# Optimization experiments

Measured on AMD Instinct MI355X. Metric: run time of the kernel, lower is better.

## Reference

```python
import jax, jax.numpy as jnp
import numpy as np

N = 262144
C = 81
NUM_HARD = 32768


def setup_inputs() -> dict:
    key = jax.random.key(0)
    k1, k2, k3, k4 = jax.random.split(key, 4)
    return {
        "cls_score": jax.random.normal(k1, (N, C), dtype=jnp.float32),
        "rois_label": jax.random.randint(k2, (N,), 0, C, dtype=jnp.int32),
        "bbox_pred": jax.random.normal(k3, (N, 4), dtype=jnp.float32),
        "rois_target": jax.random.normal(k4, (N, 4), dtype=jnp.float32),
        "rois_inside_ws": jnp.ones((N, 4), dtype=jnp.float32),
        "rois_outside_ws": jnp.ones((N, 4), dtype=jnp.float32),
        "num_hard": NUM_HARD,
    }


def reference(cls_score, rois_label, bbox_pred, rois_target,
              rois_inside_ws, rois_outside_ws, num_hard):
    num_classes = cls_score.shape[1]
    pos = rois_label > 0                                   # [N] bool
    num_pos = jnp.sum(pos.astype(jnp.float32))

    # --- hard-example mining on detached scores (no grad through selection) ---
    conf_p = jax.lax.stop_gradient(cls_score)              # [N, C]
    x_max = jnp.max(conf_p)                                # global scalar max (as in torch code)
    lse = jnp.log(jnp.sum(jnp.exp(conf_p - x_max), axis=1)) + x_max   # [N]
    gathered = jnp.take_along_axis(conf_p, rois_label[:, None].astype(jnp.int32), axis=1)[:, 0]
    loss_c = lse - gathered                                # [N]
    loss_c = jnp.where(pos, jnp.float32(100.0), loss_c)    # force positives in
    _, topk_idx = jax.lax.top_k(loss_c, num_hard)          # [num_hard]

    # --- weighted cross entropy on selected hard examples ---
    weight = jnp.ones((num_classes,), dtype=jnp.float32).at[0].set(num_pos / num_hard)
    sel_logits = cls_score[topk_idx]                       # [num_hard, C]
    sel_labels = rois_label[topk_idx]                      # [num_hard]
    logp = jax.nn.log_softmax(sel_logits, axis=1)
    nll = -jnp.take_along_axis(logp, sel_labels[:, None].astype(jnp.int32), axis=1)[:, 0]
    w = weight[sel_labels]
    loss_cls = jnp.sum(w * nll) / jnp.sum(w)               # torch weighted-mean CE

    # --- smooth L1 on positive rois only (masked; mean over num_pos*4 elems) ---
    diff = bbox_pred - rois_target                         # [N, 4]
    ad = jnp.abs(diff)
    sl1 = jnp.where(ad < 1.0, 0.5 * diff * diff, ad - 0.5)
    posf = pos.astype(sl1.dtype)[:, None]
    loss_box = jnp.sum(sl1 * posf) / (num_pos * 4.0)

    return loss_cls, loss_box
```

## Files before the change

kernel.cpp:

```cpp
#include <hip/hip_runtime.h>

#define NROWS 262144
#define NCLS  81
#define NTILES 4096
#define TILE_FLOATS 5184
#define KEY100 0xC2C80000u

struct ScalarBlk {
    unsigned mode;
    unsigned num_pos;
};

__device__ __forceinline__ unsigned mono(float f) {
    unsigned u = __float_as_uint(f);
    return (u & 0x80000000u) ? ~u : (u | 0x80000000u);
}

__global__ __launch_bounds__(256) void row_kernel(
        const float* __restrict__ cls, const int* __restrict__ label,
        const float* __restrict__ bpred, const float* __restrict__ btgt,
        float* __restrict__ nll_out,
        unsigned* __restrict__ npPart, unsigned* __restrict__ ngPart,
        unsigned* __restrict__ nePart, float* __restrict__ gtPart,
        float* __restrict__ pnPart, float* __restrict__ boxPart)
{
    __shared__ float sm[TILE_FLOATS];
    __shared__ int slbl[64];
    __shared__ unsigned wnp[4], wng[4], wne[4];
    __shared__ float wgt_[4], wpn[4], wbs[4];

    const int t   = threadIdx.x;
    const int blk = blockIdx.x;

    const float4* src = (const float4*)(cls + (size_t)blk * TILE_FLOATS);
    float4* dst = (float4*)sm;
    #pragma unroll
    for (int jj = 0; jj < 5; ++jj) dst[t + 256*jj] = src[t + 256*jj];
    if (t < 16) dst[t + 1280] = src[t + 1280];
    if (t < 64) slbl[t] = label[blk*64 + t];
    __syncthreads();

    const int row = t >> 2;
    const int j   = t & 3;
    const float* rp = sm + row * NCLS;

    float s = 0.f;
    for (int i = j; i < NCLS; i += 4) s += __expf(rp[i]);
    s += __shfl_xor(s, 1);
    s += __shfl_xor(s, 2);

    unsigned pcnt = 0, gcnt = 0, ecnt = 0;
    float gtv = 0.f, pnv = 0.f;
    if (j == 0) {
        float lse = __logf(s);
        int r = blk*64 + row;
        int lbl = slbl[row];
        bool pos = lbl > 0;
        float nll = lse - rp[lbl];
        float loss_c = pos ? 100.0f : nll;
        unsigned k = mono(loss_c);
        nll_out[r] = nll;
        pcnt = pos ? 1u : 0u;
        gcnt = (k > KEY100) ? 1u : 0u;
        ecnt = (!pos && k == KEY100) ? 1u : 0u;
        gtv  = (k > KEY100) ? nll : 0.f;
        pnv  = pos ? nll : 0.f;
    }

    float bsum = 0.f;
    {
        int gi = blk*256 + t;
        float p = bpred[gi], q = btgt[gi];
        if (slbl[row] > 0) {
            float d = p - q, ad = fabsf(d);
            bsum = (ad < 1.f) ? 0.5f*d*d : ad - 0.5f;
        }
    }

    #pragma unroll
    for (int off = 32; off; off >>= 1) {
        pcnt += __shfl_xor(pcnt, off);
        gcnt += __shfl_xor(gcnt, off);
        ecnt += __shfl_xor(ecnt, off);
        gtv  += __shfl_xor(gtv, off);
        pnv  += __shfl_xor(pnv, off);
        bsum += __shfl_xor(bsum, off);
    }
    const int lane = t & 63, wid = t >> 6;
    if (lane == 0) {
        wnp[wid] = pcnt; wng[wid] = gcnt; wne[wid] = ecnt;
        wgt_[wid] = gtv; wpn[wid] = pnv; wbs[wid] = bsum;
    }
    __syncthreads();
    if (t == 0) {
        npPart[blk]  = wnp[0]+wnp[1]+wnp[2]+wnp[3];
        ngPart[blk]  = wng[0]+wng[1]+wng[2]+wng[3];
        nePart[blk]  = wne[0]+wne[1]+wne[2]+wne[3];
        gtPart[blk]  = wgt_[0]+wgt_[1]+wgt_[2]+wgt_[3];
        pnPart[blk]  = wpn[0]+wpn[1]+wpn[2]+wpn[3];
        boxPart[blk] = wbs[0]+wbs[1]+wbs[2]+wbs[3];
    }
}

__global__ __launch_bounds__(1024) void fast_finalize(
        const unsigned* __restrict__ npPart, const unsigned* __restrict__ ngPart,
        const unsigned* __restrict__ nePart, const float* __restrict__ gtPart,
        const float* __restrict__ pnPart, const float* __restrict__ boxPart,
        const int* __restrict__ label, const float* __restrict__ nll,
        const int* __restrict__ d_num_hard, ScalarBlk* __restrict__ sc,
        float* __restrict__ out)
{
    const int t = threadIdx.x, lane = t & 63, wid = t >> 6;
    __shared__ unsigned wNp[16], wNg[16], wNe[16];
    __shared__ float wPn[16], wGt[16], wBx[16];
    __shared__ unsigned sCross, sCumBefore;
    __shared__ float sFull, sPartial;

    uint4  np = ((const uint4*)npPart)[t];
    uint4  ng = ((const uint4*)ngPart)[t];
    uint4  ne = ((const uint4*)nePart)[t];
    float4 gt = ((const float4*)gtPart)[t];
    float4 pn = ((const float4*)pnPart)[t];
    float4 bx = ((const float4*)boxPart)[t];
    unsigned myNp = np.x+np.y+np.z+np.w;
    unsigned myNg = ng.x+ng.y+ng.z+ng.w;
    unsigned myNe = ne.x+ne.y+ne.z+ne.w;
    float myGt = gt.x+gt.y+gt.z+gt.w;
    float myPn = pn.x+pn.y+pn.z+pn.w;
    float myBx = bx.x+bx.y+bx.z+bx.w;

    unsigned incNp = myNp; float incPn = myPn;
    #pragma unroll
    for (int off = 1; off < 64; off <<= 1) {
        unsigned v = __shfl_up(incNp, off);
        float    f = __shfl_up(incPn, off);
        if (lane >= off) { incNp += v; incPn += f; }
    }
    #pragma unroll
    for (int off = 32; off; off >>= 1) {
        myNg += __shfl_xor(myNg, off);
        myNe += __shfl_xor(myNe, off);
        myGt += __shfl_xor(myGt, off);
        myBx += __shfl_xor(myBx, off);
    }
    if (lane == 63) { wNp[wid] = incNp; wPn[wid] = incPn; }
    if (lane == 0)  { wNg[wid] = myNg; wNe[wid] = myNe; wGt[wid] = myGt; wBx[wid] = myBx; }
    __syncthreads();

    unsigned NP = 0, NG = 0, NE = 0; float GT = 0.f, BX = 0.f;
    unsigned npOff = 0; float pnOff = 0.f;
    for (int w = 0; w < 16; ++w) {
        NP += wNp[w]; NG += wNg[w]; NE += wNe[w]; GT += wGt[w]; BX += wBx[w];
        if (w < wid) { npOff += wNp[w]; pnOff += wPn[w]; }
    }
    const unsigned k = (unsigned)(*d_num_hard);
    const bool fast = (NG < k) && (NG + NP >= k) && (NE == 0);
    if (t == 0) { sc->mode = fast ? 1u : 0u; sc->num_pos = NP; }

    if (fast) {
        const unsigned need = k - NG;
        unsigned E = npOff + incNp - myNp;
        float    F = pnOff + incPn - myPn;
        unsigned a[4] = { np.x, np.y, np.z, np.w };
        float    p4[4] = { pn.x, pn.y, pn.z, pn.w };
        unsigned cum = E; float fl = F;
        #pragma unroll
        for (int i = 0; i < 4; ++i) {
            if (cum < need && cum + a[i] >= need) {
                sCross = (unsigned)(4*t + i); sCumBefore = cum; sFull = fl;
            }
            cum += a[i]; fl += p4[i];
        }
    }
    __syncthreads();
    if (!fast) return;

    const unsigned need = k - NG;
    if (t < 64) {
        int r = (int)sCross * 64 + t;
        int lbl = label[r];
        float v = nll[r];
        bool pos = lbl > 0;
        unsigned long long b = __ballot(pos);
        unsigned rank = (unsigned)__popcll(b & ((1ull << t) - 1ull));
        unsigned rem = need - sCumBefore;
        float c = (pos && rank < rem) ? v : 0.f;
        #pragma unroll
        for (int off = 32; off; off >>= 1) c += __shfl_xor(c, off);
        if (t == 0) sPartial = c;
    }
    __syncthreads();
    if (t == 0) {
        float wgt0 = (float)NP / (float)k;
        float num = wgt0 * GT + sFull + sPartial;
        float den = wgt0 * (float)NG + (float)need;
        out[0] = num / den;
        out[1] = BX / ((float)NP * 4.0f);
    }
}

__device__ void scan_desc_64k(const unsigned* hist, unsigned k,
                              unsigned* outB, unsigned* outRem,
                              unsigned* wsum )
{
    const int t = threadIdx.x, lane = t & 63, wid = t >> 6;
    unsigned sum = 0;
    for (int j = 0; j < 64; ++j) sum += hist[65535 - (t*64 + j)];
    unsigned inc = sum;
    #pragma unroll
    for (int off = 1; off < 64; off <<= 1) {
        unsigned v = __shfl_up(inc, off);
        if (lane >= off) inc += v;
    }
    if (lane == 63) wsum[wid] = inc;
    __syncthreads();
    unsigned woff = 0;
    for (int w = 0; w < wid; ++w) woff += wsum[w];
    unsigned running = woff + inc - sum;
    for (int j = 0; j < 64; ++j) {
        unsigned bkt = 65535u - (unsigned)(t*64 + j);
        unsigned c = hist[bkt];
        if (running < k && running + c >= k) { *outB = bkt; *outRem = k - running; }
        running += c;
    }
}

__global__ __launch_bounds__(1024) void slow_fallback(
        const int* __restrict__ label, const float* __restrict__ nll,
        const float* __restrict__ boxPart, const int* __restrict__ d_num_hard,
        const ScalarBlk* __restrict__ sc, unsigned* __restrict__ hist,
        float* __restrict__ out)
{
    if (sc->mode) return;
    const int t = threadIdx.x, lane = t & 63, wid = t >> 6;
    const unsigned k = (unsigned)(*d_num_hard);
    const unsigned NP = sc->num_pos;
    __shared__ unsigned wsum[16];
    __shared__ unsigned sB1, sKrem, sTkey, sNeed;
    __shared__ unsigned wEq[16];
    __shared__ float r1[16], r2[16], r3[16];

    for (int i = t; i < 65536; i += 1024) hist[i] = 0u;
    __syncthreads();
    for (int base = 0; base < NROWS; base += 1024) {
        int r = base + t;
        int lbl = label[r]; float v = nll[r];
        unsigned key = mono(lbl > 0 ? 100.0f : v);
        unsigned bkt = key >> 16;
        unsigned long long active = __ballot(1);
        while (active) {
            int leader = (int)__builtin_ctzll(active);
            unsigned lb = __shfl(bkt, leader);
            unsigned long long grp = __ballot(bkt == lb) & active;
            if (lane == leader) atomicAdd(&hist[lb], (unsigned)__popcll(grp));
            active &= ~grp;
        }
    }
    __syncthreads();
    scan_desc_64k(hist, k, &sB1, &sKrem, wsum);
    __syncthreads();

    for (int i = t; i < 65536; i += 1024) hist[i] = 0u;
    __syncthreads();
    for (int base = 0; base < NROWS; base += 1024) {
        int r = base + t;
        int lbl = label[r]; float v = nll[r];
        unsigned key = mono(lbl > 0 ? 100.0f : v);
        bool in = (key >> 16) == sB1;
        unsigned bkt = key & 0xFFFFu;
        unsigned long long active = __ballot(in);
        while (active) {
            int leader = (int)__builtin_ctzll(active);
            unsigned lb = __shfl(bkt, leader);
            unsigned long long grp = __ballot(in && bkt == lb) & active;
            if (lane == leader) atomicAdd(&hist[lb], (unsigned)__popcll(grp));
            active &= ~grp;
        }
    }
    __syncthreads();
    scan_desc_64k(hist, sKrem, &sTkey, &sNeed, wsum);
    __syncthreads();
    if (t == 0) sTkey = (sB1 << 16) | sTkey;
    __syncthreads();

    const unsigned tkey = sTkey, need = sNeed;
    const float wgt0 = (float)NP / (float)k;
    float accN = 0.f, accW = 0.f;
    unsigned running = 0;
    for (int base = 0; base < NROWS; base += 1024) {
        int r = base + t;
        int lbl = label[r]; float v = nll[r];
        unsigned key = mono(lbl > 0 ? 100.0f : v);
        bool eq = (key == tkey);
        unsigned long long b = __ballot(eq);
        if (lane == 0) wEq[wid] = (unsigned)__popcll(b);
        __syncthreads();
        unsigned woff = 0, chunkTotal = 0;
        for (int w = 0; w < 16; ++w) {
            chunkTotal += wEq[w];
            if (w < wid) woff += wEq[w];
        }
        unsigned rank = running + woff + (unsigned)__popcll(b & ((1ull << lane) - 1ull));
        bool sel = (key > tkey) || (eq && rank < need);
        if (sel) { float wg = (lbl == 0) ? wgt0 : 1.f; accN += wg * v; accW += wg; }
        running += chunkTotal;
        __syncthreads();
    }
    float bx = 0.f;
    for (int i = t; i < NTILES; i += 1024) bx += boxPart[i];
    #pragma unroll
    for (int off = 32; off; off >>= 1) {
        accN += __shfl_xor(accN, off);
        accW += __shfl_xor(accW, off);
        bx   += __shfl_xor(bx, off);
    }
    if (lane == 0) { r1[wid] = accN; r2[wid] = accW; r3[wid] = bx; }
    __syncthreads();
    if (t == 0) {
        float N = 0.f, W = 0.f, B = 0.f;
        for (int w = 0; w < 16; ++w) { N += r1[w]; W += r2[w]; B += r3[w]; }
        out[0] = N / W;
        out[1] = B / ((float)NP * 4.0f);
    }
}

extern "C" void kernel_launch(void* const* d_in, const int* in_sizes, int n_in,
                              void* d_out, int out_size, void* d_ws, size_t ws_size,
                              hipStream_t stream) {
    const float* cls   = (const float*)d_in[0];
    const int*   label = (const int*)d_in[1];
    const float* bpred = (const float*)d_in[2];
    const float* btgt  = (const float*)d_in[3];
    const int*   nh    = (const int*)d_in[6];
    float* out = (float*)d_out;

    char* ws = (char*)d_ws;
    ScalarBlk* sc      = (ScalarBlk*)(ws);
    unsigned*  npPart  = (unsigned*)(ws + 4096);
    unsigned*  ngPart  = (unsigned*)(ws + 4096 + 16384*1);
    unsigned*  nePart  = (unsigned*)(ws + 4096 + 16384*2);
    float*     gtPart  = (float*)(ws + 4096 + 16384*3);
    float*     pnPart  = (float*)(ws + 4096 + 16384*4);
    float*     boxPart = (float*)(ws + 4096 + 16384*5);
    float*     nll     = (float*)(ws + 4096 + 16384*6);
    unsigned*  hist    = (unsigned*)(ws + 4096 + 16384*6 + 1048576);

    row_kernel<<<NTILES, 256, 0, stream>>>(cls, label, bpred, btgt, nll,
                                           npPart, ngPart, nePart,
                                           gtPart, pnPart, boxPart);
    fast_finalize<<<1, 1024, 0, stream>>>(npPart, ngPart, nePart, gtPart,
                                          pnPart, boxPart, label, nll, nh,
                                          sc, out);
    slow_fallback<<<1, 1024, 0, stream>>>(label, nll, boxPart, nh, sc, hist, out);
}
```

Measured before the change: 31.26 us.

## Merge finalize and fallback kernels, pack per-tile partials, drop global nll buffer

The row kernel stops writing a per-row nll array and instead packs its per-tile counts and sums into a single float4 (three 8-bit counts bit-packed into one lane). The fast-path finalize and the slow fallback become one kernel, removing one launch. In the fast path that kernel recomputes nll only for the single crossing tile from cls. The slow path now recomputes nll for every row serially inside a single block, which makes that path much more expensive, and the bit-packing assumes each per-tile count fits in 8 bits (at most 64 rows per tile).

```diff
diff --git a/kernel.cpp b/kernel.cpp
--- a/kernel.cpp
+++ b/kernel.cpp
@@ -6,11 +6,6 @@
 #define TILE_FLOATS 5184
 #define KEY100 0xC2C80000u
 
-struct ScalarBlk {
-    unsigned mode;
-    unsigned num_pos;
-};
-
 __device__ __forceinline__ unsigned mono(float f) {
     unsigned u = __float_as_uint(f);
     return (u & 0x80000000u) ? ~u : (u | 0x80000000u);
@@ -19,31 +14,40 @@
 __global__ __launch_bounds__(256) void row_kernel(
         const float* __restrict__ cls, const int* __restrict__ label,
         const float* __restrict__ bpred, const float* __restrict__ btgt,
-        float* __restrict__ nll_out,
-        unsigned* __restrict__ npPart, unsigned* __restrict__ ngPart,
-        unsigned* __restrict__ nePart, float* __restrict__ gtPart,
-        float* __restrict__ pnPart, float* __restrict__ boxPart)
+        float4* __restrict__ partial)
 {
     __shared__ float sm[TILE_FLOATS];
     __shared__ int slbl[64];
-    __shared__ unsigned wnp[4], wng[4], wne[4];
-    __shared__ float wgt_[4], wpn[4], wbs[4];
-
-    const int t   = threadIdx.x;
+    __shared__ unsigned ru[3][4];
+    __shared__ float rf[3][4];
+
+    const int t = threadIdx.x;
+    const int lane = t & 63, wid = t >> 6;
     const int blk = blockIdx.x;
-
-    const float4* src = (const float4*)(cls + (size_t)blk * TILE_FLOATS);
-    float4* dst = (float4*)sm;
-    #pragma unroll
-    for (int jj = 0; jj < 5; ++jj) dst[t + 256*jj] = src[t + 256*jj];
-    if (t < 16) dst[t + 1280] = src[t + 1280];
+    const int row = t >> 2, j = t & 3;
+
+    int myLbl = label[blk*64 + row];
     if (t < 64) slbl[t] = label[blk*64 + t];
-    __syncthreads();
-
-    const int row = t >> 2;
-    const int j   = t & 3;
+    float bsum = 0.f;
+    {
+        int gi = blk*256 + t;
+        float p = bpred[gi], q = btgt[gi];
+        if (myLbl > 0) {
+            float d = p - q, ad = fabsf(d);
+            bsum = (ad < 1.f) ? 0.5f*d*d : ad - 0.5f;
+        }
+    }
+
+    {
+        const float4* src = (const float4*)(cls + (size_t)blk * TILE_FLOATS);
+        float4* dst = (float4*)sm;
+        #pragma unroll
+        for (int jj = 0; jj < 5; ++jj) dst[t + 256*jj] = src[t + 256*jj];
+        if (t < 16) dst[t + 1280] = src[t + 1280];
+    }
+    __syncthreads();
+
     const float* rp = sm + row * NCLS;
-
     float s = 0.f;
     for (int i = j; i < NCLS; i += 4) s += __expf(rp[i]);
     s += __shfl_xor(s, 1);
@@ -53,30 +57,15 @@
     float gtv = 0.f, pnv = 0.f;
     if (j == 0) {
         float lse = __logf(s);
-        int r = blk*64 + row;
-        int lbl = slbl[row];
-        bool pos = lbl > 0;
-        float nll = lse - rp[lbl];
-        float loss_c = pos ? 100.0f : nll;
-        unsigned k = mono(loss_c);
-        nll_out[r] = nll;
+        bool pos = myLbl > 0;
+        float nll = lse - rp[myLbl];
+        unsigned kk = mono(pos ? 100.0f : nll);
         pcnt = pos ? 1u : 0u;
-        gcnt = (k > KEY100) ? 1u : 0u;
-        ecnt = (!pos && k == KEY100) ? 1u : 0u;
-        gtv  = (k > KEY100) ? nll : 0.f;
+        gcnt = (kk > KEY100) ? 1u : 0u;
+        ecnt = (!pos && kk == KEY100) ? 1u : 0u;
+        gtv  = (kk > KEY100) ? nll : 0.f;
         pnv  = pos ? nll : 0.f;
     }
-
-    float bsum = 0.f;
-    {
-        int gi = blk*256 + t;
-        float p = bpred[gi], q = btgt[gi];
-        if (slbl[row] > 0) {
-            float d = p - q, ad = fabsf(d);
-            bsum = (ad < 1.f) ? 0.5f*d*d : ad - 0.5f;
-        }
-    }
-
     #pragma unroll
     for (int off = 32; off; off >>= 1) {
         pcnt += __shfl_xor(pcnt, off);
@@ -86,122 +75,25 @@
         pnv  += __shfl_xor(pnv, off);
         bsum += __shfl_xor(bsum, off);
     }
-    const int lane = t & 63, wid = t >> 6;
     if (lane == 0) {
-        wnp[wid] = pcnt; wng[wid] = gcnt; wne[wid] = ecnt;
-        wgt_[wid] = gtv; wpn[wid] = pnv; wbs[wid] = bsum;
+        ru[0][wid] = pcnt; ru[1][wid] = gcnt; ru[2][wid] = ecnt;
+        rf[0][wid] = gtv;  rf[1][wid] = pnv;  rf[2][wid] = bsum;
     }
     __syncthreads();
     if (t == 0) {
-        npPart[blk]  = wnp[0]+wnp[1]+wnp[2]+wnp[3];
-        ngPart[blk]  = wng[0]+wng[1]+wng[2]+wng[3];
-        nePart[blk]  = wne[0]+wne[1]+wne[2]+wne[3];
-        gtPart[blk]  = wgt_[0]+wgt_[1]+wgt_[2]+wgt_[3];
-        pnPart[blk]  = wpn[0]+wpn[1]+wpn[2]+wpn[3];
-        boxPart[blk] = wbs[0]+wbs[1]+wbs[2]+wbs[3];
-    }
-}
-
-__global__ __launch_bounds__(1024) void fast_finalize(
-        const unsigned* __restrict__ npPart, const unsigned* __restrict__ ngPart,
-        const unsigned* __restrict__ nePart, const float* __restrict__ gtPart,
-        const float* __restrict__ pnPart, const float* __restrict__ boxPart,
-        const int* __restrict__ label, const float* __restrict__ nll,
-        const int* __restrict__ d_num_hard, ScalarBlk* __restrict__ sc,
-        float* __restrict__ out)
-{
-    const int t = threadIdx.x, lane = t & 63, wid = t >> 6;
-    __shared__ unsigned wNp[16], wNg[16], wNe[16];
-    __shared__ float wPn[16], wGt[16], wBx[16];
-    __shared__ unsigned sCross, sCumBefore;
-    __shared__ float sFull, sPartial;
-
-    uint4  np = ((const uint4*)npPart)[t];
-    uint4  ng = ((const uint4*)ngPart)[t];
-    uint4  ne = ((const uint4*)nePart)[t];
-    float4 gt = ((const float4*)gtPart)[t];
-    float4 pn = ((const float4*)pnPart)[t];
-    float4 bx = ((const float4*)boxPart)[t];
-    unsigned myNp = np.x+np.y+np.z+np.w;
-    unsigned myNg = ng.x+ng.y+ng.z+ng.w;
-    unsigned myNe = ne.x+ne.y+ne.z+ne.w;
-    float myGt = gt.x+gt.y+gt.z+gt.w;
-    float myPn = pn.x+pn.y+pn.z+pn.w;
-    float myBx = bx.x+bx.y+bx.z+bx.w;
-
-    unsigned incNp = myNp; float incPn = myPn;
-    #pragma unroll
-    for (int off = 1; off < 64; off <<= 1) {
-        unsigned v = __shfl_up(incNp, off);
-        float    f = __shfl_up(incPn, off);
-        if (lane >= off) { incNp += v; incPn += f; }
-    }
-    #pragma unroll
-    for (int off = 32; off; off >>= 1) {
-        myNg += __shfl_xor(myNg, off);
-        myNe += __shfl_xor(myNe, off);
-        myGt += __shfl_xor(myGt, off);
-        myBx += __shfl_xor(myBx, off);
-    }
-    if (lane == 63) { wNp[wid] = incNp; wPn[wid] = incPn; }
-    if (lane == 0)  { wNg[wid] = myNg; wNe[wid] = myNe; wGt[wid] = myGt; wBx[wid] = myBx; }
-    __syncthreads();
-
-    unsigned NP = 0, NG = 0, NE = 0; float GT = 0.f, BX = 0.f;
-    unsigned npOff = 0; float pnOff = 0.f;
-    for (int w = 0; w < 16; ++w) {
-        NP += wNp[w]; NG += wNg[w]; NE += wNe[w]; GT += wGt[w]; BX += wBx[w];
-        if (w < wid) { npOff += wNp[w]; pnOff += wPn[w]; }
-    }
-    const unsigned k = (unsigned)(*d_num_hard);
-    const bool fast = (NG < k) && (NG + NP >= k) && (NE == 0);
-    if (t == 0) { sc->mode = fast ? 1u : 0u; sc->num_pos = NP; }
-
-    if (fast) {
-        const unsigned need = k - NG;
-        unsigned E = npOff + incNp - myNp;
-        float    F = pnOff + incPn - myPn;
-        unsigned a[4] = { np.x, np.y, np.z, np.w };
-        float    p4[4] = { pn.x, pn.y, pn.z, pn.w };
-        unsigned cum = E; float fl = F;
-        #pragma unroll
-        for (int i = 0; i < 4; ++i) {
-            if (cum < need && cum + a[i] >= need) {
-                sCross = (unsigned)(4*t + i); sCumBefore = cum; sFull = fl;
-            }
-            cum += a[i]; fl += p4[i];
-        }
-    }
-    __syncthreads();
-    if (!fast) return;
-
-    const unsigned need = k - NG;
-    if (t < 64) {
-        int r = (int)sCross * 64 + t;
-        int lbl = label[r];
-        float v = nll[r];
-        bool pos = lbl > 0;
-        unsigned long long b = __ballot(pos);
-        unsigned rank = (unsigned)__popcll(b & ((1ull << t) - 1ull));
-        unsigned rem = need - sCumBefore;
-        float c = (pos && rank < rem) ? v : 0.f;
-        #pragma unroll
-        for (int off = 32; off; off >>= 1) c += __shfl_xor(c, off);
-        if (t == 0) sPartial = c;
-    }
-    __syncthreads();
-    if (t == 0) {
-        float wgt0 = (float)NP / (float)k;
-        float num = wgt0 * GT + sFull + sPartial;
-        float den = wgt0 * (float)NG + (float)need;
-        out[0] = num / den;
-        out[1] = BX / ((float)NP * 4.0f);
-    }
-}
-
-__device__ void scan_desc_64k(const unsigned* hist, unsigned k,
-                              unsigned* outB, unsigned* outRem,
-                              unsigned* wsum )
+        unsigned np = ru[0][0]+ru[0][1]+ru[0][2]+ru[0][3];
+        unsigned ng = ru[1][0]+ru[1][1]+ru[1][2]+ru[1][3];
+        unsigned ne = ru[2][0]+ru[2][1]+ru[2][2]+ru[2][3];
+        float gt = rf[0][0]+rf[0][1]+rf[0][2]+rf[0][3];
+        float pn = rf[1][0]+rf[1][1]+rf[1][2]+rf[1][3];
+        float bx = rf[2][0]+rf[2][1]+rf[2][2]+rf[2][3];
+        partial[blk] = make_float4(__uint_as_float(np | (ng<<8) | (ne<<16)), gt, pn, bx);
+    }
+}
+
+__device__ void scan_desc_64k_1024(const unsigned* hist, unsigned k,
+                                   unsigned* outB, unsigned* outRem,
+                                   unsigned* wsum )
 {
     const int t = threadIdx.x, lane = t & 63, wid = t >> 6;
     unsigned sum = 0;
@@ -225,27 +117,131 @@
     }
 }
 
-__global__ __launch_bounds__(1024) void slow_fallback(
-        const int* __restrict__ label, const float* __restrict__ nll,
-        const float* __restrict__ boxPart, const int* __restrict__ d_num_hard,
-        const ScalarBlk* __restrict__ sc, unsigned* __restrict__ hist,
+__global__ __launch_bounds__(1024) void finalize_kernel(
+        const float* __restrict__ cls, const int* __restrict__ label,
+        const float4* __restrict__ partial, const int* __restrict__ d_num_hard,
+        unsigned* __restrict__ hist, float* __restrict__ nllbuf,
         float* __restrict__ out)
 {
-    if (sc->mode) return;
     const int t = threadIdx.x, lane = t & 63, wid = t >> 6;
+    __shared__ unsigned wNp[16], wNg[16], wNe[16];
+    __shared__ float wPn[16], wGt[16], wBx[16];
+    __shared__ unsigned sCross, sCumBefore;
+    __shared__ float sFull, sPartial;
+    __shared__ float sm[TILE_FLOATS];
+    __shared__ float snll[64];
+    __shared__ int slbl[64];
+
+    unsigned npI[4]; float pnI[4];
+    unsigned npS = 0, ngS = 0, neS = 0;
+    float gtS = 0.f, pnS = 0.f, bxS = 0.f;
+    #pragma unroll
+    for (int i = 0; i < 4; ++i) {
+        float4 v = partial[t*4 + i];
+        unsigned c = __float_as_uint(v.x);
+        npI[i] = c & 255u; pnI[i] = v.z;
+        npS += npI[i]; ngS += (c >> 8) & 255u; neS += (c >> 16) & 255u;
+        gtS += v.y; pnS += v.z; bxS += v.w;
+    }
+    unsigned incNp = npS; float incPn = pnS;
+    #pragma unroll
+    for (int off = 1; off < 64; off <<= 1) {
+        unsigned v = __shfl_up(incNp, off);
+        float    f = __shfl_up(incPn, off);
+        if (lane >= off) { incNp += v; incPn += f; }
+    }
+    #pragma unroll
+    for (int off = 32; off; off >>= 1) {
+        ngS += __shfl_xor(ngS, off); neS += __shfl_xor(neS, off);
+        gtS += __shfl_xor(gtS, off); bxS += __shfl_xor(bxS, off);
+    }
+    if (lane == 63) { wNp[wid] = incNp; wPn[wid] = incPn; }
+    if (lane == 0)  { wNg[wid] = ngS; wNe[wid] = neS; wGt[wid] = gtS; wBx[wid] = bxS; }
+    __syncthreads();
+
+    unsigned NP = 0, NG = 0, NE = 0; float GT = 0.f, BX = 0.f;
+    unsigned npOff = 0; float pnOff = 0.f;
+    for (int w = 0; w < 16; ++w) {
+        NP += wNp[w]; NG += wNg[w]; NE += wNe[w]; GT += wGt[w]; BX += wBx[w];
+        if (w < wid) { npOff += wNp[w]; pnOff += wPn[w]; }
+    }
     const unsigned k = (unsigned)(*d_num_hard);
-    const unsigned NP = sc->num_pos;
+    const bool fast = (NG < k) && (NG + NP >= k) && (NE == 0);
+
+    if (fast) {
+        const unsigned need = k - NG;
+        unsigned cum = npOff + incNp - npS;
+        float    fl  = pnOff + incPn - pnS;
+        #pragma unroll
+        for (int i = 0; i < 4; ++i) {
+            if (cum < need && cum + npI[i] >= need) {
+                sCross = (unsigned)(t*4 + i); sCumBefore = cum; sFull = fl;
+            }
+            cum += npI[i]; fl += pnI[i];
+        }
+        __syncthreads();
+
+        {
+            const float4* src = (const float4*)(cls + (size_t)sCross * TILE_FLOATS);
+            float4* dst = (float4*)sm;
+            dst[t] = src[t];
+            if (t < 272) dst[t + 1024] = src[t + 1024];
+            if (t < 64) slbl[t] = label[(int)sCross*64 + t];
+        }
+        __syncthreads();
+
+        {
+            const int brow = t >> 4, bj = t & 15;
+            const float* rp = sm + brow * NCLS;
+            float s = 0.f;
+            for (int i = bj; i < NCLS; i += 16) s += __expf(rp[i]);
+            s += __shfl_xor(s, 1);
+            s += __shfl_xor(s, 2);
+            s += __shfl_xor(s, 4);
+            s += __shfl_xor(s, 8);
+            if (bj == 0) snll[brow] = __logf(s) - rp[slbl[brow]];
+        }
+        __syncthreads();
+
+        if (t < 64) {
+            int lbl = slbl[t];
+            bool pos = lbl > 0;
+            unsigned long long m = __ballot(pos);
+            unsigned rank = (unsigned)__popcll(m & ((1ull << t) - 1ull));
+            unsigned rem = need - sCumBefore;
+            float c = (pos && rank < rem) ? snll[t] : 0.f;
+            #pragma unroll
+            for (int off = 32; off; off >>= 1) c += __shfl_xor(c, off);
+            if (t == 0) sPartial = c;
+        }
+        __syncthreads();
+        if (t == 0) {
+            float wgt0 = (float)NP / (float)k;
+            out[0] = (wgt0*GT + sFull + sPartial) / (wgt0*NG + (float)need);
+            out[1] = BX / ((float)NP * 4.0f);
+        }
+        return;
+    }
+
     __shared__ unsigned wsum[16];
     __shared__ unsigned sB1, sKrem, sTkey, sNeed;
     __shared__ unsigned wEq[16];
-    __shared__ float r1[16], r2[16], r3[16];
+    __shared__ float r1[16], r2[16];
+    __syncthreads();
+
+    for (int r = t; r < NROWS; r += 1024) {
+        const float* rp = cls + (size_t)r * NCLS;
+        float ssum = 0.f;
+        for (int cix = 0; cix < NCLS; ++cix) ssum += __expf(rp[cix]);
+        nllbuf[r] = __logf(ssum) - rp[label[r]];
+    }
+    __syncthreads();
 
     for (int i = t; i < 65536; i += 1024) hist[i] = 0u;
     __syncthreads();
     for (int base = 0; base < NROWS; base += 1024) {
         int r = base + t;
-        int lbl = label[r]; float v = nll[r];
-        unsigned key = mono(lbl > 0 ? 100.0f : v);
+        unsigned key = mono(label[r] > 0 ? 100.0f : nllbuf[r]);
         unsigned bkt = key >> 16;
         unsigned long long active = __ballot(1);
         while (active) {
@@ -257,15 +253,14 @@
         }
     }
     __syncthreads();
-    scan_desc_64k(hist, k, &sB1, &sKrem, wsum);
+    scan_desc_64k_1024(hist, k, &sB1, &sKrem, wsum);
     __syncthreads();
 
     for (int i = t; i < 65536; i += 1024) hist[i] = 0u;
     __syncthreads();
     for (int base = 0; base < NROWS; base += 1024) {
         int r = base + t;
-        int lbl = label[r]; float v = nll[r];
-        unsigned key = mono(lbl > 0 ? 100.0f : v);
+        unsigned key = mono(label[r] > 0 ? 100.0f : nllbuf[r]);
         bool in = (key >> 16) == sB1;
         unsigned bkt = key & 0xFFFFu;
         unsigned long long active = __ballot(in);
@@ -278,7 +273,7 @@
         }
     }
     __syncthreads();
-    scan_desc_64k(hist, sKrem, &sTkey, &sNeed, wsum);
+    scan_desc_64k_1024(hist, sKrem, &sTkey, &sNeed, wsum);
     __syncthreads();
     if (t == 0) sTkey = (sB1 << 16) | sTkey;
     __syncthreads();
@@ -289,7 +284,7 @@
     unsigned running = 0;
     for (int base = 0; base < NROWS; base += 1024) {
         int r = base + t;
-        int lbl = label[r]; float v = nll[r];
+        int lbl = label[r]; float v = nllbuf[r];
         unsigned key = mono(lbl > 0 ? 100.0f : v);
         bool eq = (key == tkey);
         unsigned long long b = __ballot(eq);
@@ -306,21 +301,18 @@
         running += chunkTotal;
         __syncthreads();
     }
-    float bx = 0.f;
-    for (int i = t; i < NTILES; i += 1024) bx += boxPart[i];
     #pragma unroll
     for (int off = 32; off; off >>= 1) {
         accN += __shfl_xor(accN, off);
         accW += __shfl_xor(accW, off);
-        bx   += __shfl_xor(bx, off);
-    }
-    if (lane == 0) { r1[wid] = accN; r2[wid] = accW; r3[wid] = bx; }
+    }
+    if (lane == 0) { r1[wid] = accN; r2[wid] = accW; }
     __syncthreads();
     if (t == 0) {
-        float N = 0.f, W = 0.f, B = 0.f;
-        for (int w = 0; w < 16; ++w) { N += r1[w]; W += r2[w]; B += r3[w]; }
+        float N = 0.f, W = 0.f;
+        for (int w = 0; w < 16; ++w) { N += r1[w]; W += r2[w]; }
         out[0] = N / W;
-        out[1] = B / ((float)NP * 4.0f);
+        out[1] = BX / ((float)NP * 4.0f);
     }
 }
 
@@ -335,21 +327,11 @@
     float* out = (float*)d_out;
 
     char* ws = (char*)d_ws;
-    ScalarBlk* sc      = (ScalarBlk*)(ws);
-    unsigned*  npPart  = (unsigned*)(ws + 4096);
-    unsigned*  ngPart  = (unsigned*)(ws + 4096 + 16384*1);
-    unsigned*  nePart  = (unsigned*)(ws + 4096 + 16384*2);
-    float*     gtPart  = (float*)(ws + 4096 + 16384*3);
-    float*     pnPart  = (float*)(ws + 4096 + 16384*4);
-    float*     boxPart = (float*)(ws + 4096 + 16384*5);
-    float*     nll     = (float*)(ws + 4096 + 16384*6);
-    unsigned*  hist    = (unsigned*)(ws + 4096 + 16384*6 + 1048576);
-
-    row_kernel<<<NTILES, 256, 0, stream>>>(cls, label, bpred, btgt, nll,
-                                           npPart, ngPart, nePart,
-                                           gtPart, pnPart, boxPart);
-    fast_finalize<<<1, 1024, 0, stream>>>(npPart, ngPart, nePart, gtPart,
-                                          pnPart, boxPart, label, nll, nh,
-                                          sc, out);
-    slow_fallback<<<1, 1024, 0, stream>>>(label, nll, boxPart, nh, sc, hist, out);
-}
+    float4*   partial = (float4*)(ws);
+    unsigned* hist    = (unsigned*)(ws + 65536);
+    float*    nllbuf  = (float*)(ws + 65536 + 262144);
+
+    row_kernel<<<NTILES, 256, 0, stream>>>(cls, label, bpred, btgt, partial);
+    finalize_kernel<<<1, 1024, 0, stream>>>(cls, label, partial, nh,
+                                            hist, nllbuf, out);
+}
```

Result: faster. 29.15 us, median of 2 (-6.7%).
